# Performance work log

Hardware: AMD Instinct MI355X
Metric: run time of the kernel (lower is better)

## Reference

```python
import jax, jax.numpy as jnp
import numpy as np
import math

B, S, E, H = 2, 2048, 768, 12
D = E // H            # head_dim = 64
FFN = 3072            # GeGLU hidden
WIN = 64              # local window size
GLOBAL_IDS = np.array([0])
EPS = 1e-5


def _rope(x):
    # x: [B,H,S,D]; interleaved rotary embedding, theta=10000 (lucidrains RotaryEmbedding)
    d = x.shape[-1]
    s = x.shape[-2]
    inv_freq = 1.0 / (10000.0 ** (jnp.arange(0, d, 2, dtype=jnp.float32) / d))
    freqs = jnp.arange(s, dtype=jnp.float32)[:, None] * inv_freq[None, :]  # [S, D/2]
    freqs = jnp.repeat(freqs, 2, axis=-1)                                   # [S, D]
    cos, sin = jnp.cos(freqs), jnp.sin(freqs)
    xp = x.reshape(x.shape[:-1] + (d // 2, 2))
    x_rot = jnp.stack([-xp[..., 1], xp[..., 0]], axis=-1).reshape(x.shape)
    return x * cos + x_rot * sin


def _layernorm(x, scale, bias):
    mu = jnp.mean(x, axis=-1, keepdims=True)
    var = jnp.mean(jnp.square(x - mu), axis=-1, keepdims=True)
    return (x - mu) * jax.lax.rsqrt(var + EPS) * scale + bias


def setup_inputs() -> dict:
    key = jax.random.key(0)
    ks = jax.random.split(key, 10)
    def xav(k, shape, gain):
        fan_out, fan_in = shape
        std = gain * math.sqrt(2.0 / (fan_in + fan_out))
        return jax.random.normal(k, shape, jnp.float32) * std
    g2 = math.sqrt(2.0)
    g13 = math.sqrt(1.0 / 3.0)
    return {
        "x": jax.random.normal(ks[0], (B, S, E), jnp.float32),
        "rel_pos_bias": jax.random.normal(ks[1], (B, S, S), jnp.float32),
        "mask": jnp.ones((B, S), dtype=bool),
        "wq_w": xav(ks[2], (E, E), g2), "wq_b": jnp.zeros((E,), jnp.float32),
        "wk_w": xav(ks[3], (E, E), g2), "wk_b": jnp.zeros((E,), jnp.float32),
        "wv_w": xav(ks[4], (E, E), g2), "wv_b": jnp.zeros((E,), jnp.float32),
        "fc_w": xav(ks[5], (E, E), g2), "fc_b": jnp.zeros((E,), jnp.float32),
        "pos_coeff": jnp.full((H, 1, 1), 0.01, jnp.float32),
        "gate_w": xav(ks[6], (FFN, E), g13), "gate_b": jnp.zeros((FFN,), jnp.float32),
        "value_w": xav(ks[7], (FFN, E), g2), "value_b": jnp.zeros((FFN,), jnp.float32),
        "down_w": xav(ks[8], (E, FFN), g2), "down_b": jnp.zeros((E,), jnp.float32),
        "ln1_s": jnp.ones((E,), jnp.float32), "ln1_b": jnp.zeros((E,), jnp.float32),
        "ln2_s": jnp.ones((E,), jnp.float32), "ln2_b": jnp.zeros((E,), jnp.float32),
    }


def _sparse_allow(mask):
    # static local-window + global-token pattern, [S,S] bool
    idx = jnp.arange(S)
    allow = jnp.abs(idx[:, None] - idx[None, :]) <= WIN
    gidx = jnp.asarray(GLOBAL_IDS)
    allow = allow.at[gidx, :].set(True)
    allow = allow.at[:, gidx].set(True)
    # combine with padding mask [B,S] broadcast over query rows
    return allow[None, None, :, :] & mask[:, None, None, :]  # [B,1,S,S]


def reference(x, rel_pos_bias, mask, wq_w, wq_b, wk_w, wk_b, wv_w, wv_b,
              fc_w, fc_b, pos_coeff, gate_w, gate_b, value_w, value_b,
              down_w, down_b, ln1_s, ln1_b, ln2_s, ln2_b):
    def heads(t):  # [B,S,E] -> [B,H,S,D]
        return t.reshape(B, S, H, D).transpose(0, 2, 1, 3)

    Q = _rope(heads(x @ wq_w.T + wq_b))
    K = _rope(heads(x @ wk_w.T + wk_b))
    V = heads(x @ wv_w.T + wv_b)

    scores = jnp.einsum('bhqd,bhkd->bhqk', Q, K) / math.sqrt(D)
    scores = scores + pos_coeff[None] * rel_pos_bias[:, None]     # [B,H,S,S]
    allow = _sparse_allow(mask)
    scores = jnp.where(allow, scores, -1e30)
    scores = scores - jnp.max(scores, axis=-1, keepdims=True)
    attn = jax.nn.softmax(scores, axis=-1)
    ctx = jnp.einsum('bhqk,bhkd->bhqd', attn, V)
    ctx = ctx.transpose(0, 2, 1, 3).reshape(B, S, E)
    attn_out = ctx @ fc_w.T + fc_b

    h = _layernorm(x + attn_out, ln1_s, ln1_b)
    gate = jax.nn.gelu(h @ gate_w.T + gate_b, approximate=False)
    ffn = (gate * (h @ value_w.T + value_b)) @ down_w.T + down_b
    return _layernorm(h + ffn, ln2_s, ln2_b)
```

## Files before the change

### kernel.cpp

```cpp
#include <hip/hip_runtime.h>
#include <math.h>

#define B_   2
#define S_   2048
#define E_   768
#define H_   12
#define D_   64
#define FFN_ 3072
#define WIN_ 64
#define MTOT (B_*S_)

typedef unsigned short ushort_t;
typedef unsigned short ushort8 __attribute__((ext_vector_type(8)));
typedef __bf16 bf16x8 __attribute__((ext_vector_type(8)));
typedef float f32x4 __attribute__((ext_vector_type(4)));
typedef _Float16 half_t;

__device__ __forceinline__ float b2f(ushort_t u) {
    union { unsigned int i; float f; } c; c.i = ((unsigned int)u) << 16; return c.f;
}
__device__ __forceinline__ ushort_t f2b(float f) {
    union { float f; unsigned int i; } c; c.f = f;
    unsigned int u = c.i;
    return (ushort_t)((u + 0x7fffu + ((u >> 16) & 1u)) >> 16);
}
__device__ __forceinline__ float gelu_f(float g) {
    return 0.5f * g * (1.f + erff(g * 0.70710678118654752440f));
}

typedef const __attribute__((address_space(1))) void* gptr_t;
typedef __attribute__((address_space(3))) void* lptr_t;
__device__ __forceinline__ void gload16(const void* g, void* l) {
    __builtin_amdgcn_global_load_lds((gptr_t)g,
        (lptr_t)(unsigned int)(unsigned long long)l, 16, 0, 0);
}

__global__ __launch_bounds__(256)
void cvt_f32_bf16(const float* __restrict__ in, ushort_t* __restrict__ out, int n8)
{
    const int idx = blockIdx.x * 256 + threadIdx.x;
    if (idx >= n8) return;
    const float4* p = (const float4*)(in + (size_t)idx * 8);
    const float4 a = p[0], b = p[1];
    ushort8 o;
    o[0]=f2b(a.x); o[1]=f2b(a.y); o[2]=f2b(a.z); o[3]=f2b(a.w);
    o[4]=f2b(b.x); o[5]=f2b(b.y); o[6]=f2b(b.z); o[7]=f2b(b.w);
    *(ushort8*)(out + (size_t)idx*8) = o;
}

__global__ __launch_bounds__(256)
void cvt_interleave(const float* __restrict__ gw, const float* __restrict__ vw,
                    ushort_t* __restrict__ out)
{
    const int idx = blockIdx.x*256 + threadIdx.x;
    const int R   = idx / 96, c8 = idx - R*96;
    const int blk = R >> 6, w = R & 63;
    const float* src = (w < 32 ? gw : vw) + (size_t)(blk*32 + (w & 31))*768 + c8*8;
    const float4 a = ((const float4*)src)[0], b = ((const float4*)src)[1];
    ushort8 o;
    o[0]=f2b(a.x); o[1]=f2b(a.y); o[2]=f2b(a.z); o[3]=f2b(a.w);
    o[4]=f2b(b.x); o[5]=f2b(b.y); o[6]=f2b(b.z); o[7]=f2b(b.w);
    *(ushort8*)(out + (size_t)idx*8) = o;
}

__global__ __launch_bounds__(256)
void rope_table(float2* __restrict__ ctab)
{
    const int idx = blockIdx.x*256 + threadIdx.x;
    if (idx >= S_*32) return;
    const int s = idx >> 5, i = idx & 31;
    const float inv = exp2f(-(float)i * (13.287712379549449f/32.0f));
    const float fr = (float)s * inv;
    ctab[idx] = make_float2(cosf(fr), sinf(fr));
}

__global__ __launch_bounds__(256)
void rope_apply(ushort_t* __restrict__ Qb, ushort_t* __restrict__ Kb,
                const float2* __restrict__ ctab)
{
    const int NP4 = MTOT*E_/8;
    int idx = blockIdx.x*256 + threadIdx.x;
    ushort_t* ptr = Qb;
    if (idx >= NP4) { ptr = Kb; idx -= NP4; if (idx >= NP4) return; }
    const size_t p0 = (size_t)idx * 4;
    const int e2 = (int)(p0 % (E_/2));
    const int s  = (int)((p0 / (E_/2)) % S_);
    const int i0 = e2 & 31;
    ushort8 v = *(ushort8*)(ptr + p0*2);
    ushort8 o;
#pragma unroll
    for (int t = 0; t < 4; ++t) {
        const float2 cs = ctab[s*32 + i0 + t];
        const float x0 = b2f(v[2*t]), x1 = b2f(v[2*t+1]);
        o[2*t]   = f2b(x0*cs.x - x1*cs.y);
        o[2*t+1] = f2b(x1*cs.x + x0*cs.y);
    }
    *(ushort8*)(ptr + p0*2) = o;
}

template<int EPI, int BN>
__global__ __launch_bounds__(256)
void gemm_mfma(const ushort_t* __restrict__ A,
               const ushort_t* W0, const float* b0, void* C0,
               const ushort_t* W1, const float* b1, void* C1,
               const ushort_t* W2, const float* b2, void* C2,
               const void* __restrict__ aux, int M, int N, int K)
{
    constexpr int NWC = BN/64, NWR = 4/NWC, WROWS = 128/NWR, MF = WROWS/16;
    const ushort_t* W = W0; const float* bias = b0; void* C = C0;
    if (blockIdx.z == 1) { W = W1; bias = b1; C = C1; }
    else if (blockIdx.z == 2) { W = W2; bias = b2; C = C2; }

    __shared__ __align__(16) ushort_t As[128*32];
    __shared__ __align__(16) ushort_t Bs[BN*32];

    const int tid = threadIdx.x, wv = tid>>6, lane = tid&63;
    const int m0 = blockIdx.y*128, n0 = blockIdx.x*BN;
    const int wr = wv / NWC, wc = wv % NWC;
    const int lr16 = lane & 15, lkb = (lane>>4)<<3;

    f32x4 acc[MF][4];
#pragma unroll
    for (int i=0;i<MF;++i)
#pragma unroll
        for (int j=0;j<4;++j) acc[i][j] = f32x4{0.f,0.f,0.f,0.f};

    const char* Ab = (const char*)(A + (size_t)m0*K);
    const char* Wb = (const char*)(W + (size_t)n0*K);
    const size_t rb = (size_t)K*2;
    const int wbase = wv*1024, lby = lane*16;

    for (int kt = 0; kt < K; kt += 32) {
        const size_t kb = (size_t)kt*2;
        int n_ = wbase + lby;
        gload16(Ab + (size_t)(n_>>6)*rb + kb + (n_&63), (char*)As + wbase);
        n_ += 4096;
        gload16(Ab + (size_t)(n_>>6)*rb + kb + (n_&63), (char*)As + wbase + 4096);
        n_ = wbase + lby;
        gload16(Wb + (size_t)(n_>>6)*rb + kb + (n_&63), (char*)Bs + wbase);
        if (BN == 128) {
            n_ += 4096;
            gload16(Wb + (size_t)(n_>>6)*rb + kb + (n_&63), (char*)Bs + wbase + 4096);
        }
        __syncthreads();
        bf16x8 af[MF], bfr[4];
#pragma unroll
        for (int mf=0; mf<MF; ++mf)
            af[mf] = *(const bf16x8*)&As[(wr*WROWS + mf*16 + lr16)*32 + lkb];
#pragma unroll
        for (int nf=0; nf<4; ++nf)
            bfr[nf] = *(const bf16x8*)&Bs[(wc*64 + nf*16 + lr16)*32 + lkb];
#pragma unroll
        for (int mf=0; mf<MF; ++mf)
#pragma unroll
            for (int nf=0; nf<4; ++nf)
                acc[mf][nf] = __builtin_amdgcn_mfma_f32_16x16x32_bf16(af[mf], bfr[nf], acc[mf][nf], 0,0,0);
        __syncthreads();
    }

    const int colb = n0 + wc*64 + lr16;
    const int rowb = m0 + wr*WROWS + ((lane>>4)<<2);
#pragma unroll
    for (int nf=0; nf<4; ++nf) {
        const int col = colb + nf*16;
        const float bsv = bias[col];
#pragma unroll
        for (int mf=0; mf<MF; ++mf) {
            const int row = rowb + mf*16;
            const f32x4 a = acc[mf][nf];
#pragma unroll
            for (int r=0; r<4; ++r) {
                const size_t off = (size_t)(row+r)*N + col;
                const float v = a[r] + bsv;
                if constexpr (EPI == 0) {
                    ((ushort_t*)C)[off] = f2b(v);
                } else if constexpr (EPI == 1) {
                    ((float*)C)[off] = v + ((const float*)aux)[off];
                } else {
                    if (blockIdx.z == 2) {
                        const int rr = row + r;
                        const size_t toff =
                            (((size_t)(rr >> 11)*H_ + (col >> 6))*64 + (col & 63))*(size_t)S_ + (rr & (S_-1));
                        ((ushort_t*)C)[toff] = f2b(v);
                    } else {
                        ((ushort_t*)C)[off] = f2b(v);
                    }
                }
            }
        }
    }
}

__global__ __launch_bounds__(256, 3)
void gemm_geglu(const ushort_t* __restrict__ A,
                const ushort_t* __restrict__ Wgv,
                const float* __restrict__ bgp,
                const float* __restrict__ bvp,
                ushort_t* __restrict__ C)
{
    constexpr int NT   = 24;
    constexpr int ABY  = 128*64;
    constexpr int BUFB = 2*ABY;
    __shared__ __align__(16) char lds[3*BUFB];

    const int id  = blockIdx.x;
    const int stI = (id & 7)*3 + ((id >> 3) >> 6);
    const int w64 = (id >> 3) & 63;
    const int gy  = (stI/6)*8 + (w64 >> 3);
    const int gx  = (stI%6)*8 + (w64 & 7);
    const int m0 = gy*128, n0 = gx*128;

    const int tid = threadIdx.x, wv = tid>>6, l = tid&63;
    const int wr = wv>>1, wc = wv&1;
    const int lr16 = l & 15;
    const int ck = (((l>>4) ^ ((lr16>>1)&3)) << 4);

    const int lr4   = l >> 2;
    const int sslot = ((l & 3) ^ ((l >> 3) & 3)) << 4;
    const char* Agp = (const char*)A   + (size_t)(m0 + wv*32 + lr4)*1536 + sslot;
    const char* Bgp = (const char*)Wgv + (size_t)(n0 + wv*32 + lr4)*1536 + sslot;

    const int rA0 = (wr*64 +  0 + lr16)*64, rA1 = (wr*64 + 16 + lr16)*64;
    const int rA2 = (wr*64 + 32 + lr16)*64, rA3 = (wr*64 + 48 + lr16)*64;
    const int rB0 = ABY + (wc*64 +  0 + lr16)*64, rB1 = ABY + (wc*64 + 16 + lr16)*64;
    const int rB2 = ABY + (wc*64 + 32 + lr16)*64, rB3 = ABY + (wc*64 + 48 + lr16)*64;

    f32x4 acc[4][4];
#pragma unroll
    for (int i=0;i<4;++i)
#pragma unroll
        for (int j=0;j<4;++j) acc[i][j] = f32x4{0.f,0.f,0.f,0.f};

#define STG(tt, cb) { \
    char* dA = lds + (cb)*BUFB + wv*2048; \
    char* dB = lds + (cb)*BUFB + ABY + wv*2048; \
    const size_t ko = (size_t)(tt)*64; \
    gload16(Agp + ko,           dA); \
    gload16(Agp + ko + 16*1536, dA + 1024); \
    gload16(Bgp + ko,           dB); \
    gload16(Bgp + ko + 16*1536, dB + 1024); }

    STG(0, 0);
    STG(1, 1);
    asm volatile("s_waitcnt vmcnt(4)" ::: "memory");
    __builtin_amdgcn_s_barrier();

    int c = 0;
#pragma unroll 1
    for (int t = 0; t < NT; ++t) {
        const char* Lb = lds + c*BUFB;
        const int cs = (c==0) ? 2 : c-1;

        const bf16x8 a0 = *(const bf16x8*)(Lb + rA0 + ck);
        const bf16x8 a1 = *(const bf16x8*)(Lb + rA1 + ck);
        const bf16x8 a2 = *(const bf16x8*)(Lb + rA2 + ck);
        const bf16x8 a3 = *(const bf16x8*)(Lb + rA3 + ck);
        const bf16x8 b0 = *(const bf16x8*)(Lb + rB0 + ck);
        const bf16x8 b1 = *(const bf16x8*)(Lb + rB1 + ck);
        const bf16x8 b2 = *(const bf16x8*)(Lb + rB2 + ck);
        const bf16x8 b3 = *(const bf16x8*)(Lb + rB3 + ck);

        if (t < NT-2) STG(t+2, cs);

        __builtin_amdgcn_s_setprio(1);
        acc[0][0] = __builtin_amdgcn_mfma_f32_16x16x32_bf16(a0, b0, acc[0][0], 0,0,0);
        acc[1][0] = __builtin_amdgcn_mfma_f32_16x16x32_bf16(a1, b0, acc[1][0], 0,0,0);
        acc[2][0] = __builtin_amdgcn_mfma_f32_16x16x32_bf16(a2, b0, acc[2][0], 0,0,0);
        acc[3][0] = __builtin_amdgcn_mfma_f32_16x16x32_bf16(a3, b0, acc[3][0], 0,0,0);
        acc[0][1] = __builtin_amdgcn_mfma_f32_16x16x32_bf16(a0, b1, acc[0][1], 0,0,0);
        acc[1][1] = __builtin_amdgcn_mfma_f32_16x16x32_bf16(a1, b1, acc[1][1], 0,0,0);
        acc[2][1] = __builtin_amdgcn_mfma_f32_16x16x32_bf16(a2, b1, acc[2][1], 0,0,0);
        acc[3][1] = __builtin_amdgcn_mfma_f32_16x16x32_bf16(a3, b1, acc[3][1], 0,0,0);
        acc[0][2] = __builtin_amdgcn_mfma_f32_16x16x32_bf16(a0, b2, acc[0][2], 0,0,0);
        acc[1][2] = __builtin_amdgcn_mfma_f32_16x16x32_bf16(a1, b2, acc[1][2], 0,0,0);
        acc[2][2] = __builtin_amdgcn_mfma_f32_16x16x32_bf16(a2, b2, acc[2][2], 0,0,0);
        acc[3][2] = __builtin_amdgcn_mfma_f32_16x16x32_bf16(a3, b2, acc[3][2], 0,0,0);
        acc[0][3] = __builtin_amdgcn_mfma_f32_16x16x32_bf16(a0, b3, acc[0][3], 0,0,0);
        acc[1][3] = __builtin_amdgcn_mfma_f32_16x16x32_bf16(a1, b3, acc[1][3], 0,0,0);
        acc[2][3] = __builtin_amdgcn_mfma_f32_16x16x32_bf16(a2, b3, acc[2][3], 0,0,0);
        acc[3][3] = __builtin_amdgcn_mfma_f32_16x16x32_bf16(a3, b3, acc[3][3], 0,0,0);
        __builtin_amdgcn_s_setprio(0);

        if (t < NT-2)       { asm volatile("s_waitcnt vmcnt(4)" ::: "memory"); }
        else if (t == NT-2) { asm volatile("s_waitcnt vmcnt(0)" ::: "memory"); }
        if (t < NT-1) __builtin_amdgcn_s_barrier();

        c = (c==2) ? 0 : c+1;
    }
#undef STG

    const int colb = gx*64 + wc*32 + lr16;
    const int rowb = m0 + wr*64 + ((l>>4)<<2);
#pragma unroll
    for (int nf=0; nf<2; ++nf) {
        const int col = colb + nf*16;
        const float bgv = bgp[col], bvv = bvp[col];
#pragma unroll
        for (int mf=0; mf<4; ++mf) {
            const int row = rowb + mf*16;
            const f32x4 gq = acc[mf][nf];
            const f32x4 vq = acc[mf][nf+2];
#pragma unroll
            for (int r=0; r<4; ++r) {
                C[(size_t)(row+r)*3072 + col] =
                    f2b(gelu_f(gq[r] + bgv) * (vq[r] + bvv));
            }
        }
    }
}

__global__ __launch_bounds__(256, 3)
void gemm_down(const ushort_t* __restrict__ A,
               const ushort_t* __restrict__ Wd,
               const float* __restrict__ bias,
               float* __restrict__ P0,
               half_t* __restrict__ P1)
{
    constexpr int NT   = 24;
    constexpr int ABY  = 128*128;
    constexpr int BBY  = 64*128;
    constexpr int BUFB = ABY + BBY;
    __shared__ __align__(16) char lds[2*BUFB];

    const int id   = blockIdx.x;
    const int work = (id & 7)*96 + (id >> 3);
    const int z    = work / 384;
    const int r    = work - z*384;
    const int gy   = r / 12, gx = r - gy*12;
    const int m0 = gy*128, n0 = gx*64;

    const int tid = threadIdx.x, wv = tid>>6, l = tid&63;
    const int wr = wv>>1, wc = wv&1;
    const int lr16 = l & 15, g16b = (l>>4)<<4;
    const int xr = (lr16 & 7) << 4;

    const int lrow = l >> 3;
    const int swzc = ((l & 7) ^ lrow) << 4;
    const size_t kbase = (size_t)z*3072;
    const char* Agp = (const char*)A  + (size_t)(m0 + wv*32 + lrow)*6144 + kbase + swzc;
    const char* Bgp = (const char*)Wd + (size_t)(n0 + wv*16 + lrow)*6144 + kbase + swzc;

    const int rA0 = (wr*64 +  0 + lr16)*128, rA1 = (wr*64 + 16 + lr16)*128;
    const int rA2 = (wr*64 + 32 + lr16)*128, rA3 = (wr*64 + 48 + lr16)*128;
    const int rB0 = ABY + (wc*32 +  0 + lr16)*128;
    const int rB1 = ABY + (wc*32 + 16 + lr16)*128;
    const int ck0 = g16b ^ xr, ck1 = (64 + g16b) ^ xr;

    f32x4 acc[4][2];
#pragma unroll
    for (int i=0;i<4;++i)
#pragma unroll
        for (int j=0;j<2;++j) acc[i][j] = f32x4{0.f,0.f,0.f,0.f};

#define STGD(tt, cb) { \
    char* dA = lds + (cb)*BUFB + wv*4096; \
    char* dB = lds + (cb)*BUFB + ABY + wv*2048; \
    const size_t ko = (size_t)(tt)*128; \
    gload16(Agp + ko,           dA); \
    gload16(Agp + ko +  8*6144, dA + 1024); \
    gload16(Agp + ko + 16*6144, dA + 2048); \
    gload16(Agp + ko + 24*6144, dA + 3072); \
    gload16(Bgp + ko,           dB); \
    gload16(Bgp + ko +  8*6144, dB + 1024); }

    STGD(0, 0);
    __syncthreads();

    int c = 0;
#pragma unroll 1
    for (int t = 0; t < NT; ++t) {
        if (t < NT-1) STGD(t+1, c^1);
        const char* Lb = lds + c*BUFB;
        const bf16x8 a0 = *(const bf16x8*)(Lb + rA0 + ck0);
        const bf16x8 a1 = *(const bf16x8*)(Lb + rA1 + ck0);
        const bf16x8 a2 = *(const bf16x8*)(Lb + rA2 + ck0);
        const bf16x8 a3 = *(const bf16x8*)(Lb + rA3 + ck0);
        const bf16x8 b0 = *(const bf16x8*)(Lb + rB0 + ck0);
        const bf16x8 b1 = *(const bf16x8*)(Lb + rB1 + ck0);
        const bf16x8 e0 = *(const bf16x8*)(Lb + rA0 + ck1);
        const bf16x8 e1 = *(const bf16x8*)(Lb + rA1 + ck1);
        const bf16x8 e2 = *(const bf16x8*)(Lb + rA2 + ck1);
        const bf16x8 e3 = *(const bf16x8*)(Lb + rA3 + ck1);
        const bf16x8 f0 = *(const bf16x8*)(Lb + rB0 + ck1);
        const bf16x8 f1 = *(const bf16x8*)(Lb + rB1 + ck1);
        __builtin_amdgcn_s_setprio(1);
        acc[0][0] = __builtin_amdgcn_mfma_f32_16x16x32_bf16(a0, b0, acc[0][0], 0,0,0);
        acc[1][0] = __builtin_amdgcn_mfma_f32_16x16x32_bf16(a1, b0, acc[1][0], 0,0,0);
        acc[2][0] = __builtin_amdgcn_mfma_f32_16x16x32_bf16(a2, b0, acc[2][0], 0,0,0);
        acc[3][0] = __builtin_amdgcn_mfma_f32_16x16x32_bf16(a3, b0, acc[3][0], 0,0,0);
        acc[0][1] = __builtin_amdgcn_mfma_f32_16x16x32_bf16(a0, b1, acc[0][1], 0,0,0);
        acc[1][1] = __builtin_amdgcn_mfma_f32_16x16x32_bf16(a1, b1, acc[1][1], 0,0,0);
        acc[2][1] = __builtin_amdgcn_mfma_f32_16x16x32_bf16(a2, b1, acc[2][1], 0,0,0);
        acc[3][1] = __builtin_amdgcn_mfma_f32_16x16x32_bf16(a3, b1, acc[3][1], 0,0,0);
        acc[0][0] = __builtin_amdgcn_mfma_f32_16x16x32_bf16(e0, f0, acc[0][0], 0,0,0);
        acc[1][0] = __builtin_amdgcn_mfma_f32_16x16x32_bf16(e1, f0, acc[1][0], 0,0,0);
        acc[2][0] = __builtin_amdgcn_mfma_f32_16x16x32_bf16(e2, f0, acc[2][0], 0,0,0);
        acc[3][0] = __builtin_amdgcn_mfma_f32_16x16x32_bf16(e3, f0, acc[3][0], 0,0,0);
        acc[0][1] = __builtin_amdgcn_mfma_f32_16x16x32_bf16(e0, f1, acc[0][1], 0,0,0);
        acc[1][1] = __builtin_amdgcn_mfma_f32_16x16x32_bf16(e1, f1, acc[1][1], 0,0,0);
        acc[2][1] = __builtin_amdgcn_mfma_f32_16x16x32_bf16(e2, f1, acc[2][1], 0,0,0);
        acc[3][1] = __builtin_amdgcn_mfma_f32_16x16x32_bf16(e3, f1, acc[3][1], 0,0,0);
        __builtin_amdgcn_s_setprio(0);
        __syncthreads();
        c ^= 1;
    }
#undef STGD

    const int colb = n0 + wc*32 + lr16;
    const int rowb = m0 + wr*64 + ((l>>4)<<2);
#pragma unroll
    for (int nf=0; nf<2; ++nf) {
        const int col = colb + nf*16;
        const float bsv = bias[col];
#pragma unroll
        for (int mf=0; mf<4; ++mf) {
            const int row = rowb + mf*16;
            const f32x4 a = acc[mf][nf];
#pragma unroll
            for (int rr=0; rr<4; ++rr) {
                const size_t off = (size_t)(row+rr)*E_ + col;
                if (z == 0) P0[off] = a[rr] + bsv;
                else        P1[off] = (half_t)a[rr];
            }
        }
    }
}

__global__ __launch_bounds__(256)
void attn_mfma(const ushort_t* __restrict__ Qb, const ushort_t* __restrict__ Kb,
               const ushort_t* __restrict__ Vt, const float* __restrict__ rel,
               const float* __restrict__ pos_coeff, ushort_t* __restrict__ ctx)
{
    __shared__ __align__(16) ushort_t P_lds[4][16][160];
    const int id = blockIdx.x;
    const int h  = id % H_;
    const int qb = (id / H_) & 31;
    const int b  = id / (H_*32);
    const int wv = threadIdx.x >> 6, l = threadIdx.x & 63;
    const int qw = qb*64 + wv*16;
    const int g  = l >> 4, ql = l & 15;
    const int q  = qw + ql;

    int klo = qw - 64;
    if (klo < 0) klo = 0;
    if (klo > S_-160) klo = S_-160;
    const bool addg = (klo > 0);
    const float pc = pos_coeff[h];

    const ushort_t* qbp = Qb + ((size_t)(b*S_ + qw))*E_ + h*D_ + (size_t)ql*E_ + g*8;
    const bf16x8 qf0 = *(const bf16x8*)(qbp);
    const bf16x8 qf1 = *(const bf16x8*)(qbp + 32);

    float sg = -1e30f, pg = 0.f;
    const float* relrow = rel + ((size_t)(b*S_ + q))*S_;
    if (addg) {
        const ushort_t* k0p = Kb + (size_t)(b*S_)*E_ + h*D_ + g*8;
        const bf16x8 k00 = *(const bf16x8*)(k0p);
        const bf16x8 k01 = *(const bf16x8*)(k0p + 32);
        float part = 0.f;
#pragma unroll
        for (int t = 0; t < 8; ++t) {
            part = fmaf((float)k00[t], (float)qf0[t], part);
            part = fmaf((float)k01[t], (float)qf1[t], part);
        }
        part += __shfl_xor(part, 16);
        part += __shfl_xor(part, 32);
        sg = part*0.125f + pc*relrow[0];
    }

    f32x4 sc_[10];
#pragma unroll
    for (int f = 0; f < 10; ++f) sc_[f] = f32x4{0.f,0.f,0.f,0.f};
    const ushort_t* kbp = Kb + ((size_t)(b*S_ + klo))*E_ + h*D_;
#pragma unroll
    for (int f = 0; f < 10; ++f) {
        const ushort_t* kr = kbp + (size_t)(16*f + ql)*E_ + g*8;
        const bf16x8 kf0 = *(const bf16x8*)(kr);
        const bf16x8 kf1 = *(const bf16x8*)(kr + 32);
        sc_[f] = __builtin_amdgcn_mfma_f32_16x16x32_bf16(kf0, qf0, sc_[f], 0,0,0);
        sc_[f] = __builtin_amdgcn_mfma_f32_16x16x32_bf16(kf1, qf1, sc_[f], 0,0,0);
    }

#pragma unroll
    for (int f = 0; f < 10; ++f) {
#pragma unroll
        for (int r = 0; r < 4; ++r) {
            const int slot = 16*f + 4*g + r;
            const int key  = klo + slot;
            const int dd   = key - q;
            const bool ok  = (dd <= WIN_ && dd >= -WIN_) || (key == 0);
            const float v  = sc_[f][r]*0.125f + pc*relrow[key];
            sc_[f][r] = ok ? v : -1e30f;
        }
    }

    float mx = sg;
#pragma unroll
    for (int f = 0; f < 10; ++f)
#pragma unroll
        for (int r = 0; r < 4; ++r) mx = fmaxf(mx, sc_[f][r]);
    mx = fmaxf(mx, __shfl_xor(mx, 16));
    mx = fmaxf(mx, __shfl_xor(mx, 32));

    float ls = 0.f;
#pragma unroll
    for (int f = 0; f < 10; ++f)
#pragma unroll
        for (int r = 0; r < 4; ++r) {
            const float p = __expf(sc_[f][r] - mx);
            sc_[f][r] = p; ls += p;
        }
    if (addg) pg = __expf(sg - mx);
    ls += (g == 0) ? pg : 0.f;
    ls += __shfl_xor(ls, 16);
    ls += __shfl_xor(ls, 32);
    const float inv = 1.f / ls;

#pragma unroll
    for (int f = 0; f < 10; ++f)
#pragma unroll
        for (int r = 0; r < 4; ++r)
            P_lds[wv][ql][16*f + 4*g + r] = f2b(sc_[f][r]);
    __syncthreads();

    f32x4 acc_c[4];
#pragma unroll
    for (int df = 0; df < 4; ++df) acc_c[df] = f32x4{0.f,0.f,0.f,0.f};
    const ushort_t* vtb = Vt + ((size_t)(b*H_ + h)*64)*(size_t)S_;
#pragma unroll
    for (int s5 = 0; s5 < 5; ++s5) {
        const bf16x8 pf = *(const bf16x8*)&P_lds[wv][ql][32*s5 + 8*g];
#pragma unroll
        for (int df = 0; df < 4; ++df) {
            const bf16x8 vtf = *(const bf16x8*)(vtb + (size_t)(df*16 + ql)*S_ + klo + 32*s5 + g*8);
            acc_c[df] = __builtin_amdgcn_mfma_f32_16x16x32_bf16(vtf, pf, acc_c[df], 0,0,0);
        }
    }

    if (addg) {
#pragma unroll
        for (int df = 0; df < 4; ++df)
#pragma unroll
            for (int r = 0; r < 4; ++r)
                acc_c[df][r] = fmaf(pg, b2f(vtb[(size_t)(df*16 + g*4 + r)*S_]), acc_c[df][r]);
    }

    if (q != 0) {
        ushort_t* cb = ctx + ((size_t)(b*S_ + q))*E_ + h*D_;
#pragma unroll
        for (int df = 0; df < 4; ++df)
#pragma unroll
            for (int r = 0; r < 4; ++r)
                cb[df*16 + g*4 + r] = f2b(acc_c[df][r] * inv);
    }
}

__global__ __launch_bounds__(256)
void attn_global(const ushort_t* __restrict__ Qb, const ushort_t* __restrict__ Kb,
                 const ushort_t* __restrict__ Vt, const float* __restrict__ rel,
                 const float* __restrict__ pos_coeff, ushort_t* __restrict__ ctx)
{
    __shared__ float sc[S_];
    __shared__ float sq[D_];
    __shared__ float red[4];
    __shared__ float pacc[4][D_];
    const int tid = threadIdx.x, wv = tid>>6, lane = tid&63;
    const int id = blockIdx.x, h = id % H_, b = id / H_;

    if (tid < 64) sq[tid] = b2f(Qb[(size_t)(b*S_)*E_ + h*D_ + tid]);
    __syncthreads();

    const float pc = pos_coeff[h];
    const ushort_t* kbase = Kb + (size_t)b*S_*E_ + h*D_;
    const float* relrow = rel + (size_t)b*S_*S_;
    const int g = lane >> 2, sl = lane & 3;

    for (int jb = wv*16; jb < S_; jb += 64) {
        const int j = jb + g;
        const ushort_t* kr = kbase + (size_t)j*E_ + sl*16;
        const ushort8 k0 = *(const ushort8*)kr;
        const ushort8 k1 = *(const ushort8*)(kr + 8);
        const float* qv = &sq[sl*16];
        float partial = 0.f;
#pragma unroll
        for (int t = 0; t < 8; ++t) partial = fmaf(b2f(k0[t]), qv[t], partial);
#pragma unroll
        for (int t = 0; t < 8; ++t) partial = fmaf(b2f(k1[t]), qv[t+8], partial);
        partial += __shfl_xor(partial, 1);
        partial += __shfl_xor(partial, 2);
        if (sl == 0) sc[j] = partial*0.125f + pc*relrow[j];
    }
    __syncthreads();

    float mx = -1e30f;
#pragma unroll
    for (int i = 0; i < 8; ++i) mx = fmaxf(mx, sc[tid + 256*i]);
#pragma unroll
    for (int off = 32; off > 0; off >>= 1) mx = fmaxf(mx, __shfl_xor(mx, off));
    if (lane == 0) red[wv] = mx;
    __syncthreads();
    mx = fmaxf(fmaxf(red[0], red[1]), fmaxf(red[2], red[3]));

    float sum = 0.f;
#pragma unroll
    for (int i = 0; i < 8; ++i) {
        const float p = __expf(sc[tid + 256*i] - mx);
        sc[tid + 256*i] = p; sum += p;
    }
#pragma unroll
    for (int off = 32; off > 0; off >>= 1) sum += __shfl_xor(sum, off);
    __syncthreads();
    if (lane == 0) red[wv] = sum;
    __syncthreads();
    const float inv = 1.f / (red[0]+red[1]+red[2]+red[3]);

    const ushort_t* vtrow = Vt + ((size_t)(b*H_ + h)*64 + lane)*(size_t)S_;
    float acc = 0.f;
    for (int j0 = wv*512; j0 < wv*512 + 512; j0 += 8) {
        const ushort8 v8 = *(const ushort8*)&vtrow[j0];
#pragma unroll
        for (int t = 0; t < 8; ++t) acc = fmaf(sc[j0+t], b2f(v8[t]), acc);
    }
    pacc[wv][lane] = acc;
    __syncthreads();
    if (tid < 64) {
        const float r = (pacc[0][tid]+pacc[1][tid]+pacc[2][tid]+pacc[3][tid]) * inv;
        ctx[(size_t)(b*S_)*E_ + h*D_ + tid] = f2b(r);
    }
}

template<bool WB>
__global__ __launch_bounds__(256)
void ln_kernel(const float* __restrict__ in, const float* __restrict__ gam,
               const float* __restrict__ bet, float* __restrict__ out,
               ushort_t* __restrict__ outb)
{
    const int row = blockIdx.x;
    const float* r = in + (size_t)row * E_;
    const int tid = threadIdx.x;
    const float v0 = r[tid], v1 = r[tid+256], v2 = r[tid+512];
    float s  = v0+v1+v2;
    float ss = v0*v0+v1*v1+v2*v2;
#pragma unroll
    for (int off = 32; off > 0; off >>= 1) {
        s  += __shfl_xor(s, off);
        ss += __shfl_xor(ss, off);
    }
    __shared__ float rs[4], rss[4];
    const int wv = tid >> 6, lane = tid & 63;
    if (lane == 0) { rs[wv] = s; rss[wv] = ss; }
    __syncthreads();
    s  = rs[0]+rs[1]+rs[2]+rs[3];
    ss = rss[0]+rss[1]+rss[2]+rss[3];
    const float mu  = s * (1.f/E_);
    const float var = ss * (1.f/E_) - mu*mu;
    const float rstd = rsqrtf(var + 1e-5f);
    float* o = out + (size_t)row * E_;
    const float o0 = (v0-mu)*rstd*gam[tid    ] + bet[tid    ];
    const float o1 = (v1-mu)*rstd*gam[tid+256] + bet[tid+256];
    const float o2 = (v2-mu)*rstd*gam[tid+512] + bet[tid+512];
    o[tid] = o0; o[tid+256] = o1; o[tid+512] = o2;
    if constexpr (WB) {
        ushort_t* ob = outb + (size_t)row * E_;
        ob[tid] = f2b(o0); ob[tid+256] = f2b(o1); ob[tid+512] = f2b(o2);
    }
}

__global__ __launch_bounds__(256)
void ln3_kernel(const float* __restrict__ p0, const half_t* __restrict__ p1,
                const float* __restrict__ res, const float* __restrict__ gam,
                const float* __restrict__ bet, float* __restrict__ out)
{
    const int row = blockIdx.x;
    const size_t base = (size_t)row * E_;
    const int tid = threadIdx.x;
    const float v0 = p0[base+tid]     + (float)p1[base+tid]     + res[base+tid];
    const float v1 = p0[base+tid+256] + (float)p1[base+tid+256] + res[base+tid+256];
    const float v2 = p0[base+tid+512] + (float)p1[base+tid+512] + res[base+tid+512];
    float s  = v0+v1+v2;
    float ss = v0*v0+v1*v1+v2*v2;
#pragma unroll
    for (int off = 32; off > 0; off >>= 1) {
        s  += __shfl_xor(s, off);
        ss += __shfl_xor(ss, off);
    }
    __shared__ float rs[4], rss[4];
    const int wv = tid >> 6, lane = tid & 63;
    if (lane == 0) { rs[wv] = s; rss[wv] = ss; }
    __syncthreads();
    s  = rs[0]+rs[1]+rs[2]+rs[3];
    ss = rss[0]+rss[1]+rss[2]+rss[3];
    const float mu  = s * (1.f/E_);
    const float var = ss * (1.f/E_) - mu*mu;
    const float rstd = rsqrtf(var + 1e-5f);
    float* o = out + base;
    o[tid]     = (v0-mu)*rstd*gam[tid    ] + bet[tid    ];
    o[tid+256] = (v1-mu)*rstd*gam[tid+256] + bet[tid+256];
    o[tid+512] = (v2-mu)*rstd*gam[tid+512] + bet[tid+512];
}

extern "C" void kernel_launch(void* const* d_in, const int* in_sizes, int n_in,
                              void* d_out, int out_size, void* d_ws, size_t ws_size,
                              hipStream_t stream)
{
    const float* x      = (const float*)d_in[0];
    const float* rel    = (const float*)d_in[1];
    const float* wq_w   = (const float*)d_in[3];
    const float* wq_b   = (const float*)d_in[4];
    const float* wk_w   = (const float*)d_in[5];
    const float* wk_b   = (const float*)d_in[6];
    const float* wv_w   = (const float*)d_in[7];
    const float* wv_b   = (const float*)d_in[8];
    const float* fc_w   = (const float*)d_in[9];
    const float* fc_b   = (const float*)d_in[10];
    const float* pos_c  = (const float*)d_in[11];
    const float* gate_w = (const float*)d_in[12];
    const float* gate_b = (const float*)d_in[13];
    const float* value_w= (const float*)d_in[14];
    const float* value_b= (const float*)d_in[15];
    const float* down_w = (const float*)d_in[16];
    const float* down_b = (const float*)d_in[17];
    const float* ln1_s  = (const float*)d_in[18];
    const float* ln1_b  = (const float*)d_in[19];
    const float* ln2_s  = (const float*)d_in[20];
    const float* ln2_b  = (const float*)d_in[21];
    float* out = (float*)d_out;

    char* W = (char*)d_ws;
    ushort_t* Qb     = (ushort_t*)(W + 0);
    ushort_t* Kb     = (ushort_t*)(W + 6291456);
    ushort_t* Vt     = (ushort_t*)(W + 12582912);
    ushort_t* Cxb    = (ushort_t*)(W + 18874368);
    ushort_t* GpB    = (ushort_t*)(W + 0);
    ushort_t* Xb     = (ushort_t*)(W + 25165824);
    ushort_t* wqb    = (ushort_t*)(W + 31457280);
    ushort_t* wkb    = (ushort_t*)(W + 32636928);
    ushort_t* wvb    = (ushort_t*)(W + 33816576);
    ushort_t* fcb    = (ushort_t*)(W + 34996224);
    ushort_t* Wgv    = (ushort_t*)(W + 25165824);
    ushort_t* downb  = (ushort_t*)(W + 34996224);
    float*    AO     = (float*)   (W + 39714816);
    float*    Hb     = (float*)   (W + 52297728);
    ushort_t* Hbb    = (ushort_t*)(W + 64880640);
    half_t*   P1h    = (half_t*)  (W + 64880640);
    float2*   ctab   = (float2*)  (W + 71172096);

    cvt_f32_bf16<<<1536, 256, 0, stream>>>(x, Xb, MTOT*E_/8);
    cvt_f32_bf16<<<288,  256, 0, stream>>>(wq_w, wqb, E_*E_/8);
    cvt_f32_bf16<<<288,  256, 0, stream>>>(wk_w, wkb, E_*E_/8);
    cvt_f32_bf16<<<288,  256, 0, stream>>>(wv_w, wvb, E_*E_/8);
    cvt_f32_bf16<<<288,  256, 0, stream>>>(fc_w, fcb, E_*E_/8);
    rope_table<<<(S_*32+255)/256, 256, 0, stream>>>(ctab);

    gemm_mfma<2,128><<<dim3(E_/128, MTOT/128, 3), 256, 0, stream>>>(
        Xb, wqb, wq_b, Qb, wkb, wk_b, Kb, wvb, wv_b, Vt, nullptr, MTOT, E_, E_);

    cvt_interleave<<<2304, 256, 0, stream>>>(gate_w, value_w, Wgv);

    rope_apply<<<3072, 256, 0, stream>>>(Qb, Kb, ctab);

    attn_mfma<<<B_*H_*(S_/64), 256, 0, stream>>>(Qb, Kb, Vt, rel, pos_c, Cxb);
    attn_global<<<B_*H_, 256, 0, stream>>>(Qb, Kb, Vt, rel, pos_c, Cxb);

    gemm_mfma<1,64><<<dim3(E_/64, MTOT/128, 1), 256, 0, stream>>>(
        Cxb, fcb, fc_b, AO, nullptr, nullptr, nullptr, nullptr, nullptr, nullptr,
        x, MTOT, E_, E_);

    cvt_f32_bf16<<<1152, 256, 0, stream>>>(down_w, downb, E_*FFN_/8);

    ln_kernel<true><<<MTOT, 256, 0, stream>>>(AO, ln1_s, ln1_b, Hb, Hbb);

    gemm_geglu<<<dim3(1536), 256, 0, stream>>>(Hbb, Wgv, gate_b, value_b, GpB);

    gemm_down<<<dim3(768), 256, 0, stream>>>(GpB, downb, down_b, AO, P1h);

    ln3_kernel<<<MTOT, 256, 0, stream>>>(AO, P1h, Hb, ln2_s, ln2_b, out);
}
```

Baseline: 243.2 us.

## Widen GeGLU GEMM tile to 128x256 with double buffering

The fused gate/value GEMM tile grows from 128x128 to 128x256, so each warp holds 4x8 accumulator fragments and each A tile is reused across twice as many columns. The grid is halved and the block-to-tile mapping is remapped per XCD. The triple-buffered pipeline with explicit vmcnt waits becomes a simpler double-buffered loop with __syncthreads, and occupancy drops from 3 to 2 blocks per CU. The aim is more compute per loaded byte, at the cost of more registers, less latency hiding, and a coarser grid that may balance poorly across CUs.

```diff
diff --git a/kernel.cpp b/kernel.cpp
--- a/kernel.cpp
+++ b/kernel.cpp
@@ -191,7 +191,7 @@
     }
 }
 
-__global__ __launch_bounds__(256, 3)
+__global__ __launch_bounds__(256, 2)
 void gemm_geglu(const ushort_t* __restrict__ A,
                 const ushort_t* __restrict__ Wgv,
                 const float* __restrict__ bgp,
@@ -200,15 +200,16 @@
 {
     constexpr int NT   = 24;
     constexpr int ABY  = 128*64;
-    constexpr int BUFB = 2*ABY;
-    __shared__ __align__(16) char lds[3*BUFB];
+    constexpr int BBY  = 256*64;
+    constexpr int BUFB = ABY + BBY;
+    __shared__ __align__(16) char lds[2*BUFB];
 
     const int id  = blockIdx.x;
-    const int stI = (id & 7)*3 + ((id >> 3) >> 6);
-    const int w64 = (id >> 3) & 63;
-    const int gy  = (stI/6)*8 + (w64 >> 3);
-    const int gx  = (stI%6)*8 + (w64 & 7);
-    const int m0 = gy*128, n0 = gx*128;
+    const int w   = id >> 3;
+    const int xcd = id & 7;
+    const int gy  = (xcd >> 2)*16 + (w & 15);
+    const int gx  = (xcd & 3)*6  + (w >> 4);
+    const int m0 = gy*128, n0 = gx*256;
 
     const int tid = threadIdx.x, wv = tid>>6, l = tid&63;
     const int wr = wv>>1, wc = wv&1;
@@ -218,92 +219,73 @@
     const int lr4   = l >> 2;
     const int sslot = ((l & 3) ^ ((l >> 3) & 3)) << 4;
     const char* Agp = (const char*)A   + (size_t)(m0 + wv*32 + lr4)*1536 + sslot;
-    const char* Bgp = (const char*)Wgv + (size_t)(n0 + wv*32 + lr4)*1536 + sslot;
-
-    const int rA0 = (wr*64 +  0 + lr16)*64, rA1 = (wr*64 + 16 + lr16)*64;
-    const int rA2 = (wr*64 + 32 + lr16)*64, rA3 = (wr*64 + 48 + lr16)*64;
-    const int rB0 = ABY + (wc*64 +  0 + lr16)*64, rB1 = ABY + (wc*64 + 16 + lr16)*64;
-    const int rB2 = ABY + (wc*64 + 32 + lr16)*64, rB3 = ABY + (wc*64 + 48 + lr16)*64;
-
-    f32x4 acc[4][4];
+    const char* Bgp = (const char*)Wgv + (size_t)(n0 + wv*64 + lr4)*1536 + sslot;
+
+    int rA[4], rB[8];
+#pragma unroll
+    for (int mf=0; mf<4; ++mf) rA[mf] = (wr*64 + mf*16 + lr16)*64;
+#pragma unroll
+    for (int nf=0; nf<8; ++nf) rB[nf] = ABY + (wc*128 + nf*16 + lr16)*64;
+
+    f32x4 acc[4][8];
 #pragma unroll
     for (int i=0;i<4;++i)
 #pragma unroll
-        for (int j=0;j<4;++j) acc[i][j] = f32x4{0.f,0.f,0.f,0.f};
+        for (int j=0;j<8;++j) acc[i][j] = f32x4{0.f,0.f,0.f,0.f};
 
 #define STG(tt, cb) { \
     char* dA = lds + (cb)*BUFB + wv*2048; \
-    char* dB = lds + (cb)*BUFB + ABY + wv*2048; \
+    char* dB = lds + (cb)*BUFB + ABY + wv*4096; \
     const size_t ko = (size_t)(tt)*64; \
     gload16(Agp + ko,           dA); \
     gload16(Agp + ko + 16*1536, dA + 1024); \
     gload16(Bgp + ko,           dB); \
-    gload16(Bgp + ko + 16*1536, dB + 1024); }
+    gload16(Bgp + ko + 16*1536, dB + 1024); \
+    gload16(Bgp + ko + 32*1536, dB + 2048); \
+    gload16(Bgp + ko + 48*1536, dB + 3072); }
 
     STG(0, 0);
-    STG(1, 1);
-    asm volatile("s_waitcnt vmcnt(4)" ::: "memory");
-    __builtin_amdgcn_s_barrier();
+    __syncthreads();
 
     int c = 0;
 #pragma unroll 1
     for (int t = 0; t < NT; ++t) {
+        if (t < NT-1) STG(t+1, c^1);
         const char* Lb = lds + c*BUFB;
-        const int cs = (c==0) ? 2 : c-1;
-
-        const bf16x8 a0 = *(const bf16x8*)(Lb + rA0 + ck);
-        const bf16x8 a1 = *(const bf16x8*)(Lb + rA1 + ck);
-        const bf16x8 a2 = *(const bf16x8*)(Lb + rA2 + ck);
-        const bf16x8 a3 = *(const bf16x8*)(Lb + rA3 + ck);
-        const bf16x8 b0 = *(const bf16x8*)(Lb + rB0 + ck);
-        const bf16x8 b1 = *(const bf16x8*)(Lb + rB1 + ck);
-        const bf16x8 b2 = *(const bf16x8*)(Lb + rB2 + ck);
-        const bf16x8 b3 = *(const bf16x8*)(Lb + rB3 + ck);
-
-        if (t < NT-2) STG(t+2, cs);
-
+        bf16x8 af[4], bf[8];
+#pragma unroll
+        for (int mf=0; mf<4; ++mf) af[mf] = *(const bf16x8*)(Lb + rA[mf] + ck);
+#pragma unroll
+        for (int nf=0; nf<8; ++nf) bf[nf] = *(const bf16x8*)(Lb + rB[nf] + ck);
         __builtin_amdgcn_s_setprio(1);
-        acc[0][0] = __builtin_amdgcn_mfma_f32_16x16x32_bf16(a0, b0, acc[0][0], 0,0,0);
-        acc[1][0] = __builtin_amdgcn_mfma_f32_16x16x32_bf16(a1, b0, acc[1][0], 0,0,0);
-        acc[2][0] = __builtin_amdgcn_mfma_f32_16x16x32_bf16(a2, b0, acc[2][0], 0,0,0);
-        acc[3][0] = __builtin_amdgcn_mfma_f32_16x16x32_bf16(a3, b0, acc[3][0], 0,0,0);
-        acc[0][1] = __builtin_amdgcn_mfma_f32_16x16x32_bf16(a0, b1, acc[0][1], 0,0,0);
-        acc[1][1] = __builtin_amdgcn_mfma_f32_16x16x32_bf16(a1, b1, acc[1][1], 0,0,0);
-        acc[2][1] = __builtin_amdgcn_mfma_f32_16x16x32_bf16(a2, b1, acc[2][1], 0,0,0);
-        acc[3][1] = __builtin_amdgcn_mfma_f32_16x16x32_bf16(a3, b1, acc[3][1], 0,0,0);
-        acc[0][2] = __builtin_amdgcn_mfma_f32_16x16x32_bf16(a0, b2, acc[0][2], 0,0,0);
-        acc[1][2] = __builtin_amdgcn_mfma_f32_16x16x32_bf16(a1, b2, acc[1][2], 0,0,0);
-        acc[2][2] = __builtin_amdgcn_mfma_f32_16x16x32_bf16(a2, b2, acc[2][2], 0,0,0);
-        acc[3][2] = __builtin_amdgcn_mfma_f32_16x16x32_bf16(a3, b2, acc[3][2], 0,0,0);
-        acc[0][3] = __builtin_amdgcn_mfma_f32_16x16x32_bf16(a0, b3, acc[0][3], 0,0,0);
-        acc[1][3] = __builtin_amdgcn_mfma_f32_16x16x32_bf16(a1, b3, acc[1][3], 0,0,0);
-        acc[2][3] = __builtin_amdgcn_mfma_f32_16x16x32_bf16(a2, b3, acc[2][3], 0,0,0);
-        acc[3][3] = __builtin_amdgcn_mfma_f32_16x16x32_bf16(a3, b3, acc[3][3], 0,0,0);
+#pragma unroll
+        for (int nf=0; nf<8; ++nf)
+#pragma unroll
+            for (int mf=0; mf<4; ++mf)
+                acc[mf][nf] = __builtin_amdgcn_mfma_f32_16x16x32_bf16(af[mf], bf[nf], acc[mf][nf], 0,0,0);
         __builtin_amdgcn_s_setprio(0);
-
-        if (t < NT-2)       { asm volatile("s_waitcnt vmcnt(4)" ::: "memory"); }
-        else if (t == NT-2) { asm volatile("s_waitcnt vmcnt(0)" ::: "memory"); }
-        if (t < NT-1) __builtin_amdgcn_s_barrier();
-
-        c = (c==2) ? 0 : c+1;
+        __syncthreads();
+        c ^= 1;
     }
 #undef STG
 
-    const int colb = gx*64 + wc*32 + lr16;
     const int rowb = m0 + wr*64 + ((l>>4)<<2);
 #pragma unroll
-    for (int nf=0; nf<2; ++nf) {
-        const int col = colb + nf*16;
-        const float bgv = bgp[col], bvv = bvp[col];
-#pragma unroll
-        for (int mf=0; mf<4; ++mf) {
-            const int row = rowb + mf*16;
-            const f32x4 gq = acc[mf][nf];
-            const f32x4 vq = acc[mf][nf+2];
-#pragma unroll
-            for (int r=0; r<4; ++r) {
-                C[(size_t)(row+r)*3072 + col] =
-                    f2b(gelu_f(gq[r] + bgv) * (vq[r] + bvv));
+    for (int h=0; h<2; ++h) {
+#pragma unroll
+        for (int nfl=0; nfl<2; ++nfl) {
+            const int col = (gx*4 + wc*2 + h)*32 + nfl*16 + lr16;
+            const float bgv = bgp[col], bvv = bvp[col];
+#pragma unroll
+            for (int mf=0; mf<4; ++mf) {
+                const int row = rowb + mf*16;
+                const f32x4 gq = acc[mf][4*h + nfl];
+                const f32x4 vq = acc[mf][4*h + 2 + nfl];
+#pragma unroll
+                for (int r=0; r<4; ++r) {
+                    C[(size_t)(row+r)*3072 + col] =
+                        f2b(gelu_f(gq[r] + bgv) * (vq[r] + bvv));
+                }
             }
         }
     }
@@ -770,7 +752,7 @@
 
     ln_kernel<true><<<MTOT, 256, 0, stream>>>(AO, ln1_s, ln1_b, Hb, Hbb);
 
-    gemm_geglu<<<dim3(1536), 256, 0, stream>>>(Hbb, Wgv, gate_b, value_b, GpB);
+    gemm_geglu<<<dim3(768), 256, 0, stream>>>(Hbb, Wgv, gate_b, value_b, GpB);
 
     gemm_down<<<dim3(768), 256, 0, stream>>>(GpB, downb, down_b, AO, P1h);
 
```

Measured after the change: 246.2 us. Within noise of the previous version (+1.2%).
